# Optimization experiments

Hardware: AMD Instinct MI355X
Metric: run time of the kernel (lower is better)

## Reference

```python
import jax, jax.numpy as jnp
import numpy as np

T, B, D, H = 512, 64, 512, 512


def setup_inputs() -> dict:
    key = jax.random.key(0)
    ks = jax.random.split(key, 7)
    stdv = 1.0 / np.sqrt(H)
    u = lambda k, shape: jax.random.uniform(k, shape, jnp.float32, -stdv, stdv)
    return {
        'x': jax.random.normal(ks[0], (T, B, D), jnp.float32),
        'h0': jax.random.normal(ks[1], (B, H), jnp.float32),
        'c0': jax.random.normal(ks[2], (B, H), jnp.float32),
        'w_ih': u(ks[3], (4 * H, D)),
        'b_ih': u(ks[4], (4 * H,)),
        'w_hh': u(ks[5], (4 * H, H)),
        'b_hh': u(ks[6], (4 * H,)),
    }


def reference(x, h0, c0, w_ih, b_ih, w_hh, b_hh):
    # One LSTM layer, forward direction, no dropout, no PackedSequence.
    # gates = Linear_ih(x_t) + Linear_hh(h_{t-1}); split into i,f,g,o along features.
    def step(carry, x_t):
        h, c = carry
        gates = x_t @ w_ih.T + b_ih + h @ w_hh.T + b_hh  # [B, 4H]
        i_g, f_g, g_g, o_g = jnp.split(gates, 4, axis=1)
        c_t = jax.nn.sigmoid(f_g) * c + jax.nn.sigmoid(i_g) * jnp.tanh(g_g)
        h_t = jax.nn.sigmoid(o_g) * jnp.tanh(c_t)
        return (h_t, c_t), h_t

    (h_last, c_last), h_all = jax.lax.scan(step, (h0, c0), x)
    # output [T, B, H], final states [B, H]
    return h_all, h_last, c_last
```

## Files before the change

kernel.cpp:

```cpp
#include <hip/hip_runtime.h>
#include <stdint.h>

#define T_STEPS 512
#define BATCH   64
#define DIM     512
#define NGROUP  4
#define WG_PER_GROUP 32
#define GB      16
#define TBH     (T_STEPS*BATCH*DIM)
#define BH      (BATCH*DIM)

typedef __attribute__((ext_vector_type(8))) short short8;
typedef __attribute__((ext_vector_type(4))) float f32x4;
typedef __attribute__((ext_vector_type(4))) unsigned int u32x4;
typedef unsigned short u16;
typedef unsigned long long u64;

__device__ __forceinline__ u16 f2bf(float f) {
  union { float f; uint32_t u; } c; c.f = f;
  uint32_t u = c.u;
  return (u16)((u + 0x7FFFu + ((u >> 16) & 1u)) >> 16);
}

__device__ __forceinline__ float fsigmoid(float x) {
  float e = __expf(-x);
  return __builtin_amdgcn_rcpf(1.f + e);
}
__device__ __forceinline__ float ftanh(float x) {
  float e = __expf(2.f * x);
  return 1.f - 2.f * __builtin_amdgcn_rcpf(e + 1.f);
}

__global__ void pack_w_kernel(const float* __restrict__ w_ih,
                              const float* __restrict__ w_hh,
                              uint4* __restrict__ wpack) {
  int j = blockIdx.x;
  for (int u = threadIdx.x; u < 8192; u += 256) {
    int w    = u >> 11;
    int kt   = (u >> 6) & 31;
    int lane = u & 63;
    int n  = w * 512 + j * 16 + (lane & 15);
    int k0 = kt * 32 + 8 * (lane >> 4);
    const float* src = (k0 < 512) ? (w_ih + (size_t)n * 512 + k0)
                                  : (w_hh + (size_t)n * 512 + (k0 - 512));
    uint32_t p0 = f2bf(src[0]) | ((uint32_t)f2bf(src[1]) << 16);
    uint32_t p1 = f2bf(src[2]) | ((uint32_t)f2bf(src[3]) << 16);
    uint32_t p2 = f2bf(src[4]) | ((uint32_t)f2bf(src[5]) << 16);
    uint32_t p3 = f2bf(src[6]) | ((uint32_t)f2bf(src[7]) << 16);
    wpack[(size_t)j * 8192 + u] = make_uint4(p0, p1, p2, p3);
  }
}

__global__ void pack_x_kernel(const float* __restrict__ x, uint4* __restrict__ xbf) {
  size_t i = (size_t)blockIdx.x * 256 + threadIdx.x;
  const float4* src = (const float4*)x + i * 2;
  float4 a = src[0], b = src[1];
  uint32_t p0 = f2bf(a.x) | ((uint32_t)f2bf(a.y) << 16);
  uint32_t p1 = f2bf(a.z) | ((uint32_t)f2bf(a.w) << 16);
  uint32_t p2 = f2bf(b.x) | ((uint32_t)f2bf(b.y) << 16);
  uint32_t p3 = f2bf(b.z) | ((uint32_t)f2bf(b.w) << 16);
  xbf[i] = make_uint4(p0, p1, p2, p3);
}

__global__ void init_h_kernel(u16* __restrict__ h_buf) {
  int i = threadIdx.x + blockIdx.x * 256;
  int row = i >> 8;
  int off = i & 255;
  int p = row >> 2, g = row & 3;
  uint32_t* dst = (uint32_t*)(h_buf + (size_t)(p * NGROUP + g) * GB * DIM) + off;
  __hip_atomic_store(dst, 0u, __ATOMIC_RELAXED, __HIP_MEMORY_SCOPE_AGENT);
}

__launch_bounds__(256, 1)
__global__ void lstm_persist(const float* __restrict__ h0, const float* __restrict__ c0,
                             const float* __restrict__ b_ih, const float* __restrict__ b_hh,
                             const uint4* __restrict__ wpack, const u16* __restrict__ xbf,
                             u16* __restrict__ h_buf, float* __restrict__ out) {
  __shared__ uint4 w_lds[8192];
  __shared__ float c_lds[4][16][16];

  const int tid  = threadIdx.x;
  const int lane = tid & 63;
  const int wv   = tid >> 6;
  const int wg   = blockIdx.x;
  const int grp  = wg >> 5;
  const int wgj  = wg & 31;
  const int B0   = grp * GB;

  for (int i = tid; i < 8192; i += 256) w_lds[i] = wpack[(size_t)wgj * 8192 + i];

  const int pb   = tid >> 4;
  const int pc   = tid & 15;
  const int colg = wgj * 16 + pc;
  float c_reg = c0[(B0 + pb) * DIM + colg];
  const float bias0 = b_ih[0*512 + colg] + b_hh[0*512 + colg];
  const float bias1 = b_ih[1*512 + colg] + b_hh[1*512 + colg];
  const float bias2 = b_ih[2*512 + colg] + b_hh[2*512 + colg];
  const float bias3 = b_ih[3*512 + colg] + b_hh[3*512 + colg];

  const int m  = lane & 15;
  const int kq = 8 * (lane >> 4);

  const short8* wl = (const short8*)w_lds;

  __syncthreads();

  {
    float h0f = h0[(B0 + pb) * DIM + colg];
    float h0n = __shfl_xor(h0f, 1);
    uint32_t both = (uint32_t)f2bf(h0f) | ((uint32_t)f2bf(h0n) << 16);
    if (pb != 0 && !(pc & 1)) {
      uint32_t* p = (uint32_t*)(h_buf + ((size_t)(0 * NGROUP + grp) * GB + pb) * DIM + colg);
      __hip_atomic_store(p, both, __ATOMIC_RELAXED, __HIP_MEMORY_SCOPE_AGENT);
    }
    f32x4 a0 = (f32x4){0.f,0.f,0.f,0.f}, a1 = (f32x4){0.f,0.f,0.f,0.f};
    const u16* xrow = xbf + (size_t)(0 * BATCH + B0 + m) * DIM;
    for (int kt = 0; kt < 16; kt += 2) {
      short8 a = *((const short8*)(xrow + kt * 32 + kq));
      a0 = __builtin_amdgcn_mfma_f32_16x16x32_bf16(a, wl[(wv*32+kt)*64+lane], a0, 0,0,0);
      short8 a2 = *((const short8*)(xrow + (kt+1) * 32 + kq));
      a1 = __builtin_amdgcn_mfma_f32_16x16x32_bf16(a2, wl[(wv*32+kt+1)*64+lane], a1, 0,0,0);
    }
    f32x4 xa = a0 + a1;

    __syncthreads();
    if (pb == 0 && !(pc & 1)) {
      uint32_t v = (both & 0xFFFEFFFEu) | 0x00010001u;
      uint32_t* p = (uint32_t*)(h_buf + (size_t)(0 * NGROUP + grp) * GB * DIM + colg);
      __hip_atomic_store(p, v, __ATOMIC_RELAXED, __HIP_MEMORY_SCOPE_AGENT);
    }

    f32x4 xacc = xa;
    for (int t = 0; t < T_STEPS; ++t) {
      const int pr = t & 1;
      const u16* tb = h_buf + (size_t)(pr * NGROUP + grp) * GB * DIM;
      const uint32_t e = 1u ^ (((uint32_t)t >> 1) & 1u);
      const uint32_t want = e ? 0x00010001u : 0u;

      {
        uint64_t pa1 = (uint64_t)tb + (uint64_t)lane * 16;
        int spins = 0;
        for (;;) {
          u32x4 s;
          asm volatile("global_load_dwordx4 %0, %1, off sc0 sc1"
                       : "=v"(s) : "v"(pa1) : "memory");
          asm volatile("s_waitcnt vmcnt(0)" ::: "memory");
          __builtin_amdgcn_sched_barrier(0);
          uint32_t andv = s.x & s.y & s.z & s.w;
          uint32_t orv  = s.x | s.y | s.z | s.w;
          uint32_t chk  = e ? (andv & 0x00010001u) : (orv & 0x00010001u);
          if (__ballot(chk == want) == ~0ull) break;
          if (++spins > (1 << 18)) break;
        }
      }

      union HU { u32x4 u; short8 s; } hq[16];
      {
        uint64_t pa2 = (uint64_t)tb + (uint64_t)(m * 1024 + (lane >> 4) * 16);
#define HLOAD(i, lit)                                                          \
        asm volatile("global_load_dwordx4 %0, %1, off offset:" lit " sc0 sc1"  \
                     : "=v"(hq[i].u) : "v"(pa2) : "memory");
        HLOAD(0,"0")    HLOAD(1,"64")   HLOAD(2,"128")  HLOAD(3,"192")
        HLOAD(4,"256")  HLOAD(5,"320")  HLOAD(6,"384")  HLOAD(7,"448")
        HLOAD(8,"512")  HLOAD(9,"576")  HLOAD(10,"640") HLOAD(11,"704")
        HLOAD(12,"768") HLOAD(13,"832") HLOAD(14,"896") HLOAD(15,"960")
#undef HLOAD
        asm volatile("s_waitcnt vmcnt(0)" ::: "memory");
        __builtin_amdgcn_sched_barrier(0);
      }

      f32x4 acc0 = xacc, acc1 = (f32x4){0.f,0.f,0.f,0.f};
      #pragma unroll
      for (int kt = 0; kt < 16; kt += 2) {
        acc0 = __builtin_amdgcn_mfma_f32_16x16x32_bf16(hq[kt].s,   wl[(wv*32+16+kt)*64+lane],   acc0, 0,0,0);
        acc1 = __builtin_amdgcn_mfma_f32_16x16x32_bf16(hq[kt+1].s, wl[(wv*32+16+kt+1)*64+lane], acc1, 0,0,0);
      }
      f32x4 acc = acc0 + acc1;

      {
        int r0 = (lane >> 4) * 4;
        c_lds[wv][r0 + 0][lane & 15] = acc[0];
        c_lds[wv][r0 + 1][lane & 15] = acc[1];
        c_lds[wv][r0 + 2][lane & 15] = acc[2];
        c_lds[wv][r0 + 3][lane & 15] = acc[3];
      }
      __syncthreads();

      float gi = fsigmoid(c_lds[0][pb][pc] + bias0);
      float gf = fsigmoid(c_lds[1][pb][pc] + bias1);
      float gg = ftanh  (c_lds[2][pb][pc] + bias2);
      float go = fsigmoid(c_lds[3][pb][pc] + bias3);
      c_reg = gf * c_reg + gi * gg;
      float h = go * ftanh(c_reg);

      if (t < T_STEPS - 1) {
        float hn = __shfl_xor(h, 1);
        uint32_t both = (uint32_t)f2bf(h) | ((uint32_t)f2bf(hn) << 16);
        if (pb != 0 && !(pc & 1)) {
          uint32_t* p = (uint32_t*)(h_buf + ((size_t)((pr ^ 1) * NGROUP + grp) * GB + pb) * DIM + colg);
          __hip_atomic_store(p, both, __ATOMIC_RELAXED, __HIP_MEMORY_SCOPE_AGENT);
        }
        __syncthreads();
        {
          const uint32_t tagw = 1u ^ ((((uint32_t)t + 1) >> 1) & 1u);
          if (pb == 0 && !(pc & 1)) {
            uint32_t v = (both & 0xFFFEFFFEu) | (tagw * 0x00010001u);
            uint32_t* p = (uint32_t*)(h_buf + (size_t)((pr ^ 1) * NGROUP + grp) * GB * DIM + colg);
            __hip_atomic_store(p, v, __ATOMIC_RELAXED, __HIP_MEMORY_SCOPE_AGENT);
          }
        }
        out[((size_t)t * BATCH + B0 + pb) * DIM + colg] = h;
        f32x4 a2_0 = (f32x4){0.f,0.f,0.f,0.f}, a2_1 = (f32x4){0.f,0.f,0.f,0.f};
        const u16* xr = xbf + (size_t)((t + 1) * BATCH + B0 + m) * DIM;
        for (int kt = 0; kt < 16; kt += 2) {
          short8 a = *((const short8*)(xr + kt * 32 + kq));
          a2_0 = __builtin_amdgcn_mfma_f32_16x16x32_bf16(a, wl[(wv*32+kt)*64+lane], a2_0, 0,0,0);
          short8 a2 = *((const short8*)(xr + (kt+1) * 32 + kq));
          a2_1 = __builtin_amdgcn_mfma_f32_16x16x32_bf16(a2, wl[(wv*32+kt+1)*64+lane], a2_1, 0,0,0);
        }
        xacc = a2_0 + a2_1;
      } else {
        out[((size_t)t * BATCH + B0 + pb) * DIM + colg] = h;
        out[TBH + (B0 + pb) * DIM + colg]      = h;
        out[TBH + BH + (B0 + pb) * DIM + colg] = c_reg;
      }
    }
  }
}

extern "C" void kernel_launch(void* const* d_in, const int* in_sizes, int n_in,
                              void* d_out, int out_size, void* d_ws, size_t ws_size,
                              hipStream_t stream) {
  (void)in_sizes; (void)n_in; (void)out_size; (void)ws_size;
  const float* x    = (const float*)d_in[0];
  const float* h0   = (const float*)d_in[1];
  const float* c0   = (const float*)d_in[2];
  const float* w_ih = (const float*)d_in[3];
  const float* b_ih = (const float*)d_in[4];
  const float* w_hh = (const float*)d_in[5];
  const float* b_hh = (const float*)d_in[6];
  float* out = (float*)d_out;

  char* ws = (char*)d_ws;
  uint4* wpack = (uint4*)ws;
  u16*   xbf   = (u16*)(ws + ((size_t)4 << 20));
  u16*   hbuf  = (u16*)(ws + ((size_t)36 << 20));

  pack_w_kernel<<<dim3(32),   dim3(256), 0, stream>>>(w_ih, w_hh, wpack);
  pack_x_kernel<<<dim3(8192), dim3(256), 0, stream>>>(x, (uint4*)xbf);
  init_h_kernel<<<dim3(8),    dim3(256), 0, stream>>>(hbuf);

  void* args[] = {(void*)&h0, (void*)&c0, (void*)&b_ih, (void*)&b_hh,
                  (void*)&wpack, (void*)&xbf, (void*)&hbuf, (void*)&out};
  hipError_t e = hipLaunchCooperativeKernel((void*)lstm_persist, dim3(NGROUP * WG_PER_GROUP),
                                            dim3(256), args, 0, stream);
  if (e != hipSuccess) {
    lstm_persist<<<dim3(NGROUP * WG_PER_GROUP), dim3(256), 0, stream>>>(
        h0, c0, b_ih, b_hh, wpack, xbf, hbuf, out);
  }
}
```

Measured before the change: 2.726 ms.

## Tag every h word and poll the full tile instead of a sentinel row

Every packed bf16 pair of the hidden state now carries the parity tag in its low mantissa bits, not just the first row. Each wave spins on the same 16 loads that fetch its h operands and checks all tags itself. This merges the separate poll round trip with the data load, drops the per-step __syncthreads that ordered sentinel writes after data writes, and removes the init kernel. In exchange, every polling iteration reloads the whole tile, which adds memory traffic while waiting. Every h value loses one mantissa bit, and without the init kernel correctness depends on leftover workspace tags not matching the expected parity.

```diff
diff --git a/kernel.cpp b/kernel.cpp
--- a/kernel.cpp
+++ b/kernel.cpp
@@ -9,12 +9,12 @@
 #define GB      16
 #define TBH     (T_STEPS*BATCH*DIM)
 #define BH      (BATCH*DIM)
+#define TAGM    0x00010001u
 
 typedef __attribute__((ext_vector_type(8))) short short8;
 typedef __attribute__((ext_vector_type(4))) float f32x4;
 typedef __attribute__((ext_vector_type(4))) unsigned int u32x4;
 typedef unsigned short u16;
-typedef unsigned long long u64;
 
 __device__ __forceinline__ u16 f2bf(float f) {
   union { float f; uint32_t u; } c; c.f = f;
@@ -62,15 +62,6 @@
   xbf[i] = make_uint4(p0, p1, p2, p3);
 }
 
-__global__ void init_h_kernel(u16* __restrict__ h_buf) {
-  int i = threadIdx.x + blockIdx.x * 256;
-  int row = i >> 8;
-  int off = i & 255;
-  int p = row >> 2, g = row & 3;
-  uint32_t* dst = (uint32_t*)(h_buf + (size_t)(p * NGROUP + g) * GB * DIM) + off;
-  __hip_atomic_store(dst, 0u, __ATOMIC_RELAXED, __HIP_MEMORY_SCOPE_AGENT);
-}
-
 __launch_bounds__(256, 1)
 __global__ void lstm_persist(const float* __restrict__ h0, const float* __restrict__ c0,
                              const float* __restrict__ b_ih, const float* __restrict__ b_hh,
@@ -108,11 +99,16 @@
   {
     float h0f = h0[(B0 + pb) * DIM + colg];
     float h0n = __shfl_xor(h0f, 1);
-    uint32_t both = (uint32_t)f2bf(h0f) | ((uint32_t)f2bf(h0n) << 16);
-    if (pb != 0 && !(pc & 1)) {
+    if (!(pc & 1)) {
+      uint32_t both = (uint32_t)f2bf(h0f) | ((uint32_t)f2bf(h0n) << 16);
+      uint32_t v = (both & ~TAGM) | TAGM;
       uint32_t* p = (uint32_t*)(h_buf + ((size_t)(0 * NGROUP + grp) * GB + pb) * DIM + colg);
-      __hip_atomic_store(p, both, __ATOMIC_RELAXED, __HIP_MEMORY_SCOPE_AGENT);
-    }
+      __hip_atomic_store(p, v, __ATOMIC_RELAXED, __HIP_MEMORY_SCOPE_AGENT);
+    }
+  }
+
+  f32x4 xacc;
+  {
     f32x4 a0 = (f32x4){0.f,0.f,0.f,0.f}, a1 = (f32x4){0.f,0.f,0.f,0.f};
     const u16* xrow = xbf + (size_t)(0 * BATCH + B0 + m) * DIM;
     for (int kt = 0; kt < 16; kt += 2) {
@@ -121,42 +117,19 @@
       short8 a2 = *((const short8*)(xrow + (kt+1) * 32 + kq));
       a1 = __builtin_amdgcn_mfma_f32_16x16x32_bf16(a2, wl[(wv*32+kt+1)*64+lane], a1, 0,0,0);
     }
-    f32x4 xa = a0 + a1;
-
-    __syncthreads();
-    if (pb == 0 && !(pc & 1)) {
-      uint32_t v = (both & 0xFFFEFFFEu) | 0x00010001u;
-      uint32_t* p = (uint32_t*)(h_buf + (size_t)(0 * NGROUP + grp) * GB * DIM + colg);
-      __hip_atomic_store(p, v, __ATOMIC_RELAXED, __HIP_MEMORY_SCOPE_AGENT);
-    }
-
-    f32x4 xacc = xa;
-    for (int t = 0; t < T_STEPS; ++t) {
-      const int pr = t & 1;
-      const u16* tb = h_buf + (size_t)(pr * NGROUP + grp) * GB * DIM;
-      const uint32_t e = 1u ^ (((uint32_t)t >> 1) & 1u);
-      const uint32_t want = e ? 0x00010001u : 0u;
-
-      {
-        uint64_t pa1 = (uint64_t)tb + (uint64_t)lane * 16;
-        int spins = 0;
-        for (;;) {
-          u32x4 s;
-          asm volatile("global_load_dwordx4 %0, %1, off sc0 sc1"
-                       : "=v"(s) : "v"(pa1) : "memory");
-          asm volatile("s_waitcnt vmcnt(0)" ::: "memory");
-          __builtin_amdgcn_sched_barrier(0);
-          uint32_t andv = s.x & s.y & s.z & s.w;
-          uint32_t orv  = s.x | s.y | s.z | s.w;
-          uint32_t chk  = e ? (andv & 0x00010001u) : (orv & 0x00010001u);
-          if (__ballot(chk == want) == ~0ull) break;
-          if (++spins > (1 << 18)) break;
-        }
-      }
-
-      union HU { u32x4 u; short8 s; } hq[16];
-      {
-        uint64_t pa2 = (uint64_t)tb + (uint64_t)(m * 1024 + (lane >> 4) * 16);
+    xacc = a0 + a1;
+  }
+
+  for (int t = 0; t < T_STEPS; ++t) {
+    const int pr = t & 1;
+    const u16* tb = h_buf + (size_t)(pr * NGROUP + grp) * GB * DIM;
+    const uint32_t e = 1u ^ (((uint32_t)t >> 1) & 1u);
+
+    union HU { u32x4 u; short8 s; } hq[16];
+    {
+      uint64_t pa2 = (uint64_t)tb + (uint64_t)(m * 1024 + (lane >> 4) * 16);
+      int spins = 0;
+      for (;;) {
 #define HLOAD(i, lit)                                                          \
         asm volatile("global_load_dwordx4 %0, %1, off offset:" lit " sc0 sc1"  \
                      : "=v"(hq[i].u) : "v"(pa2) : "memory");
@@ -167,63 +140,69 @@
 #undef HLOAD
         asm volatile("s_waitcnt vmcnt(0)" ::: "memory");
         __builtin_amdgcn_sched_barrier(0);
+        uint32_t andv = 0xFFFFFFFFu, orv = 0u;
+        #pragma unroll
+        for (int i = 0; i < 16; ++i) {
+          u32x4 v = hq[i].u;
+          andv &= v.x & v.y & v.z & v.w;
+          orv  |= v.x | v.y | v.z | v.w;
+        }
+        uint32_t ok = e ? ((andv & TAGM) == TAGM) : ((orv & TAGM) == 0u);
+        if (__ballot(ok != 0u) == ~0ull) break;
+        if (++spins > (1 << 16)) break;
       }
-
-      f32x4 acc0 = xacc, acc1 = (f32x4){0.f,0.f,0.f,0.f};
-      #pragma unroll
+      __builtin_amdgcn_sched_barrier(0);
+    }
+
+    f32x4 acc0 = xacc, acc1 = (f32x4){0.f,0.f,0.f,0.f};
+    #pragma unroll
+    for (int kt = 0; kt < 16; kt += 2) {
+      acc0 = __builtin_amdgcn_mfma_f32_16x16x32_bf16(hq[kt].s,   wl[(wv*32+16+kt)*64+lane],   acc0, 0,0,0);
+      acc1 = __builtin_amdgcn_mfma_f32_16x16x32_bf16(hq[kt+1].s, wl[(wv*32+16+kt+1)*64+lane], acc1, 0,0,0);
+    }
+    f32x4 acc = acc0 + acc1;
+
+    {
+      int r0 = (lane >> 4) * 4;
+      c_lds[wv][r0 + 0][lane & 15] = acc[0];
+      c_lds[wv][r0 + 1][lane & 15] = acc[1];
+      c_lds[wv][r0 + 2][lane & 15] = acc[2];
+      c_lds[wv][r0 + 3][lane & 15] = acc[3];
+    }
+    __syncthreads();
+
+    float gi = fsigmoid(c_lds[0][pb][pc] + bias0);
+    float gf = fsigmoid(c_lds[1][pb][pc] + bias1);
+    float gg = ftanh  (c_lds[2][pb][pc] + bias2);
+    float go = fsigmoid(c_lds[3][pb][pc] + bias3);
+    c_reg = gf * c_reg + gi * gg;
+    float h = go * ftanh(c_reg);
+
+    if (t < T_STEPS - 1) {
+      {
+        float hn = __shfl_xor(h, 1);
+        if (!(pc & 1)) {
+          uint32_t both = (uint32_t)f2bf(h) | ((uint32_t)f2bf(hn) << 16);
+          const uint32_t tagw = 1u ^ ((((uint32_t)t + 1) >> 1) & 1u);
+          uint32_t v = (both & ~TAGM) | (tagw * TAGM);
+          uint32_t* p = (uint32_t*)(h_buf + ((size_t)((pr ^ 1) * NGROUP + grp) * GB + pb) * DIM + colg);
+          __hip_atomic_store(p, v, __ATOMIC_RELAXED, __HIP_MEMORY_SCOPE_AGENT);
+        }
+      }
+      out[((size_t)t * BATCH + B0 + pb) * DIM + colg] = h;
+      f32x4 a2_0 = (f32x4){0.f,0.f,0.f,0.f}, a2_1 = (f32x4){0.f,0.f,0.f,0.f};
+      const u16* xr = xbf + (size_t)((t + 1) * BATCH + B0 + m) * DIM;
       for (int kt = 0; kt < 16; kt += 2) {
-        acc0 = __builtin_amdgcn_mfma_f32_16x16x32_bf16(hq[kt].s,   wl[(wv*32+16+kt)*64+lane],   acc0, 0,0,0);
-        acc1 = __builtin_amdgcn_mfma_f32_16x16x32_bf16(hq[kt+1].s, wl[(wv*32+16+kt+1)*64+lane], acc1, 0,0,0);
+        short8 a = *((const short8*)(xr + kt * 32 + kq));
+        a2_0 = __builtin_amdgcn_mfma_f32_16x16x32_bf16(a, wl[(wv*32+kt)*64+lane], a2_0, 0,0,0);
+        short8 a2 = *((const short8*)(xr + (kt+1) * 32 + kq));
+        a2_1 = __builtin_amdgcn_mfma_f32_16x16x32_bf16(a2, wl[(wv*32+kt+1)*64+lane], a2_1, 0,0,0);
       }
-      f32x4 acc = acc0 + acc1;
-
-      {
-        int r0 = (lane >> 4) * 4;
-        c_lds[wv][r0 + 0][lane & 15] = acc[0];
-        c_lds[wv][r0 + 1][lane & 15] = acc[1];
-        c_lds[wv][r0 + 2][lane & 15] = acc[2];
-        c_lds[wv][r0 + 3][lane & 15] = acc[3];
-      }
-      __syncthreads();
-
-      float gi = fsigmoid(c_lds[0][pb][pc] + bias0);
-      float gf = fsigmoid(c_lds[1][pb][pc] + bias1);
-      float gg = ftanh  (c_lds[2][pb][pc] + bias2);
-      float go = fsigmoid(c_lds[3][pb][pc] + bias3);
-      c_reg = gf * c_reg + gi * gg;
-      float h = go * ftanh(c_reg);
-
-      if (t < T_STEPS - 1) {
-        float hn = __shfl_xor(h, 1);
-        uint32_t both = (uint32_t)f2bf(h) | ((uint32_t)f2bf(hn) << 16);
-        if (pb != 0 && !(pc & 1)) {
-          uint32_t* p = (uint32_t*)(h_buf + ((size_t)((pr ^ 1) * NGROUP + grp) * GB + pb) * DIM + colg);
-          __hip_atomic_store(p, both, __ATOMIC_RELAXED, __HIP_MEMORY_SCOPE_AGENT);
-        }
-        __syncthreads();
-        {
-          const uint32_t tagw = 1u ^ ((((uint32_t)t + 1) >> 1) & 1u);
-          if (pb == 0 && !(pc & 1)) {
-            uint32_t v = (both & 0xFFFEFFFEu) | (tagw * 0x00010001u);
-            uint32_t* p = (uint32_t*)(h_buf + (size_t)((pr ^ 1) * NGROUP + grp) * GB * DIM + colg);
-            __hip_atomic_store(p, v, __ATOMIC_RELAXED, __HIP_MEMORY_SCOPE_AGENT);
-          }
-        }
-        out[((size_t)t * BATCH + B0 + pb) * DIM + colg] = h;
-        f32x4 a2_0 = (f32x4){0.f,0.f,0.f,0.f}, a2_1 = (f32x4){0.f,0.f,0.f,0.f};
-        const u16* xr = xbf + (size_t)((t + 1) * BATCH + B0 + m) * DIM;
-        for (int kt = 0; kt < 16; kt += 2) {
-          short8 a = *((const short8*)(xr + kt * 32 + kq));
-          a2_0 = __builtin_amdgcn_mfma_f32_16x16x32_bf16(a, wl[(wv*32+kt)*64+lane], a2_0, 0,0,0);
-          short8 a2 = *((const short8*)(xr + (kt+1) * 32 + kq));
-          a2_1 = __builtin_amdgcn_mfma_f32_16x16x32_bf16(a2, wl[(wv*32+kt+1)*64+lane], a2_1, 0,0,0);
-        }
-        xacc = a2_0 + a2_1;
-      } else {
-        out[((size_t)t * BATCH + B0 + pb) * DIM + colg] = h;
-        out[TBH + (B0 + pb) * DIM + colg]      = h;
-        out[TBH + BH + (B0 + pb) * DIM + colg] = c_reg;
-      }
+      xacc = a2_0 + a2_1;
+    } else {
+      out[((size_t)t * BATCH + B0 + pb) * DIM + colg] = h;
+      out[TBH + (B0 + pb) * DIM + colg]      = h;
+      out[TBH + BH + (B0 + pb) * DIM + colg] = c_reg;
     }
   }
 }
@@ -248,7 +227,6 @@
 
   pack_w_kernel<<<dim3(32),   dim3(256), 0, stream>>>(w_ih, w_hh, wpack);
   pack_x_kernel<<<dim3(8192), dim3(256), 0, stream>>>(x, (uint4*)xbf);
-  init_h_kernel<<<dim3(8),    dim3(256), 0, stream>>>(hbuf);
 
   void* args[] = {(void*)&h0, (void*)&c0, (void*)&b_ih, (void*)&b_hh,
                   (void*)&wpack, (void*)&xbf, (void*)&hbuf, (void*)&out};
```

After: 2.657 ms. 2.5% less time.
